# Kernel optimization log

Hardware: AMD Instinct MI355X
Metric: run time of the kernel (lower is better)

Reference implementation:

```python
import jax, jax.numpy as jnp
import numpy as np

BATCH, SEQ_LEN, HIDDEN, NUM_SENTS = 16, 4096, 1024, 32


def setup_inputs() -> dict:
    key = jax.random.key(0)
    k1, k2 = jax.random.split(key)
    last_hidden_state = jax.random.normal(k1, (BATCH, SEQ_LEN, HIDDEN), dtype=jnp.float32)
    sentence_mask = jax.random.randint(k2, (BATCH, SEQ_LEN), 0, NUM_SENTS, dtype=jnp.int64)
    return {
        "last_hidden_state": last_hidden_state,
        "sentence_mask": sentence_mask,
        "num_sents": NUM_SENTS,
    }


def reference(last_hidden_state, sentence_mask, num_sents):
    # unique sentence ids; assume ids 0..num_sents-1 all occur (static shape)
    unique_sents = jnp.arange(num_sents, dtype=sentence_mask.dtype)
    # one-hot segment membership: (batch, num_sents, seq_len)
    masks = (sentence_mask[:, None, :] == unique_sents[None, :, None])
    counts = masks.sum(axis=2).astype(last_hidden_state.dtype)  # (batch, num_sents)
    # segment-sum via contraction over seq_len -> (batch, num_sents, hidden);
    # avoids the torch (B, S, L, H) broadcasted intermediate
    sums = jnp.einsum("bsl,blh->bsh", masks.astype(last_hidden_state.dtype), last_hidden_state)
    sentence_embeddings = sums / counts[:, :, None]
    return sentence_embeddings, unique_sents
```

## Files before the change

kernel.cpp:

```cpp
#include <hip/hip_runtime.h>


#define BATCH   16
#define SEQ     4096
#define HIDDEN  1024
#define NSENT   32
#define EMB_ELEMS (BATCH * NSENT * HIDDEN)

#define CHUNK2   512
#define NCHUNK2  (HIDDEN / CHUNK2)
#define GTHREADS 128

__global__ __launch_bounds__(256) void prep_kernel(const int* __restrict__ mask,
                                                   int* __restrict__ perm,
                                                   int* __restrict__ offs,
                                                   float* __restrict__ out) {
    __shared__ int sm[SEQ];
    __shared__ int cnt[NSENT];
    __shared__ int pref[NSENT];
    __shared__ int cursor[NSENT];

    const int b   = blockIdx.x;
    const int tid = threadIdx.x;

    if (tid < NSENT) cnt[tid] = 0;
    __syncthreads();

    #pragma unroll
    for (int i = tid; i < SEQ; i += 256) {
        const int s = mask[b * SEQ + i] & (NSENT - 1);
        sm[i] = s;
        atomicAdd(&cnt[s], 1);
    }
    __syncthreads();

    if (tid == 0) {
        int run = 0;
        #pragma unroll
        for (int s = 0; s < NSENT; ++s) { pref[s] = run; run += cnt[s]; }
    }
    __syncthreads();

    if (tid < NSENT) {
        cursor[tid] = pref[tid];
        offs[b * (NSENT + 1) + tid] = pref[tid];
    }
    if (tid == 0) offs[b * (NSENT + 1) + NSENT] = SEQ;
    if (b == 0 && tid < NSENT) out[EMB_ELEMS + tid] = (float)tid;
    __syncthreads();

    for (int i = tid; i < SEQ; i += 256) {
        const int s   = sm[i];
        const int pos = atomicAdd(&cursor[s], 1);
        perm[b * SEQ + pos] = i;
    }
}

__global__ __launch_bounds__(GTHREADS) void gather_kernel(const float* __restrict__ x,
                                                          const int* __restrict__ perm,
                                                          const int* __restrict__ offs,
                                                          float* __restrict__ out) {
    __shared__ int sidx[SEQ];

    const int tid   = threadIdx.x;
    const int blk   = blockIdx.x;
    const int chunk = blk & (NCHUNK2 - 1);
    const int s     = (blk >> 1) & (NSENT - 1);
    const int b     = blk >> 6;

    const int base  = b * (NSENT + 1) + s;
    const int start = offs[base];
    const int n     = offs[base + 1] - start;

    for (int j = tid; j < n; j += GTHREADS)
        sidx[j] = perm[b * SEQ + start + j];
    __syncthreads();

    const int c0 = chunk * CHUNK2 + tid * 4;
    const float* xb = x + (size_t)b * SEQ * HIDDEN + c0;

    float ax = 0.f, ay = 0.f, az = 0.f, aw = 0.f;
    #pragma unroll 8
    for (int k = 0; k < n; ++k) {
        const float4 v = *(const float4*)(xb + (size_t)sidx[k] * HIDDEN);
        ax += v.x; ay += v.y; az += v.z; aw += v.w;
    }

    const float inv = 1.0f / (float)n;
    float4 r; r.x = ax * inv; r.y = ay * inv; r.z = az * inv; r.w = aw * inv;
    *(float4*)(out + (size_t)(b * NSENT + s) * HIDDEN + c0) = r;
}

extern "C" void kernel_launch(void* const* d_in, const int* in_sizes, int n_in,
                              void* d_out, int out_size, void* d_ws, size_t ws_size,
                              hipStream_t stream) {
    const float* x    = (const float*)d_in[0];
    const int*   mask = (const int*)d_in[1];
    float*       out  = (float*)d_out;

    int* perm = (int*)d_ws;
    int* offs = perm + BATCH * SEQ;

    prep_kernel<<<BATCH, 256, 0, stream>>>(mask, perm, offs, out);
    gather_kernel<<<BATCH * NSENT * NCHUNK2, GTHREADS, 0, stream>>>(x, perm, offs, out);
}
```

Baseline: 371.9 us.

## Fuse segment index build into gather kernel, dropping separate prep pass

Removes the per-batch prep kernel that bucketed token indices, and has each gather block scan the whole mask row itself, compacting the matching indices into shared memory with a shared atomic cursor. This eliminates one kernel launch, the serialized 16-block prep stage, and the global perm/offs round trip. In exchange, every block rescans 4096 mask entries (redundant across 64 blocks per batch), and the atomic compaction produces an unordered index list, which changes summation order and may affect cache locality.

```diff
diff --git a/kernel.cpp b/kernel.cpp
--- a/kernel.cpp
+++ b/kernel.cpp
@@ -11,56 +11,11 @@
 #define NCHUNK2  (HIDDEN / CHUNK2)
 #define GTHREADS 128
 
-__global__ __launch_bounds__(256) void prep_kernel(const int* __restrict__ mask,
-                                                   int* __restrict__ perm,
-                                                   int* __restrict__ offs,
-                                                   float* __restrict__ out) {
-    __shared__ int sm[SEQ];
-    __shared__ int cnt[NSENT];
-    __shared__ int pref[NSENT];
-    __shared__ int cursor[NSENT];
-
-    const int b   = blockIdx.x;
-    const int tid = threadIdx.x;
-
-    if (tid < NSENT) cnt[tid] = 0;
-    __syncthreads();
-
-    #pragma unroll
-    for (int i = tid; i < SEQ; i += 256) {
-        const int s = mask[b * SEQ + i] & (NSENT - 1);
-        sm[i] = s;
-        atomicAdd(&cnt[s], 1);
-    }
-    __syncthreads();
-
-    if (tid == 0) {
-        int run = 0;
-        #pragma unroll
-        for (int s = 0; s < NSENT; ++s) { pref[s] = run; run += cnt[s]; }
-    }
-    __syncthreads();
-
-    if (tid < NSENT) {
-        cursor[tid] = pref[tid];
-        offs[b * (NSENT + 1) + tid] = pref[tid];
-    }
-    if (tid == 0) offs[b * (NSENT + 1) + NSENT] = SEQ;
-    if (b == 0 && tid < NSENT) out[EMB_ELEMS + tid] = (float)tid;
-    __syncthreads();
-
-    for (int i = tid; i < SEQ; i += 256) {
-        const int s   = sm[i];
-        const int pos = atomicAdd(&cursor[s], 1);
-        perm[b * SEQ + pos] = i;
-    }
-}
-
-__global__ __launch_bounds__(GTHREADS) void gather_kernel(const float* __restrict__ x,
-                                                          const int* __restrict__ perm,
-                                                          const int* __restrict__ offs,
-                                                          float* __restrict__ out) {
+__global__ __launch_bounds__(GTHREADS) void fused_kernel(const float* __restrict__ x,
+                                                         const int* __restrict__ mask,
+                                                         float* __restrict__ out) {
     __shared__ int sidx[SEQ];
+    __shared__ int cursor;
 
     const int tid   = threadIdx.x;
     const int blk   = blockIdx.x;
@@ -68,13 +23,17 @@
     const int s     = (blk >> 1) & (NSENT - 1);
     const int b     = blk >> 6;
 
-    const int base  = b * (NSENT + 1) + s;
-    const int start = offs[base];
-    const int n     = offs[base + 1] - start;
+    if (tid == 0) cursor = 0;
+    __syncthreads();
 
-    for (int j = tid; j < n; j += GTHREADS)
-        sidx[j] = perm[b * SEQ + start + j];
+    const int* mrow = mask + b * SEQ;
+    for (int i = tid; i < SEQ; i += GTHREADS) {
+        if ((mrow[i] & (NSENT - 1)) == s) {
+            sidx[atomicAdd(&cursor, 1)] = i;
+        }
+    }
     __syncthreads();
+    const int n = cursor;
 
     const int c0 = chunk * CHUNK2 + tid * 4;
     const float* xb = x + (size_t)b * SEQ * HIDDEN + c0;
@@ -89,6 +48,8 @@
     const float inv = 1.0f / (float)n;
     float4 r; r.x = ax * inv; r.y = ay * inv; r.z = az * inv; r.w = aw * inv;
     *(float4*)(out + (size_t)(b * NSENT + s) * HIDDEN + c0) = r;
+
+    if (blk == 0 && tid < NSENT) out[EMB_ELEMS + tid] = (float)tid;
 }
 
 extern "C" void kernel_launch(void* const* d_in, const int* in_sizes, int n_in,
@@ -98,9 +59,5 @@
     const int*   mask = (const int*)d_in[1];
     float*       out  = (float*)d_out;
 
-    int* perm = (int*)d_ws;
-    int* offs = perm + BATCH * SEQ;
-
-    prep_kernel<<<BATCH, 256, 0, stream>>>(mask, perm, offs, out);
-    gather_kernel<<<BATCH * NSENT * NCHUNK2, GTHREADS, 0, stream>>>(x, perm, offs, out);
+    fused_kernel<<<BATCH * NSENT * NCHUNK2, GTHREADS, 0, stream>>>(x, mask, out);
 }
```

New measurement: 373.8 us. About the same (+0.5%).
